# Kernel optimization log

Hardware: AMD Instinct MI355X
Metric: run time of the kernel (lower is better)

## Reference

```python
import jax, jax.numpy as jnp
import numpy as np

N_HEADS = 16
HEAD_DIM = 64
DIM = 1024
B, L = 2, 2048


def setup_inputs() -> dict:
    key = jax.random.key(0)
    ks = jax.random.split(key, 6)
    s = 1.0 / np.sqrt(DIM)
    return {
        "X": jax.random.normal(ks[0], (B, L, DIM), dtype=jnp.float32),
        "attention_mask": jax.random.randint(ks[1], (B, L, L), 0, 2, dtype=jnp.int32),
        "Wq": jax.random.normal(ks[2], (DIM, DIM), dtype=jnp.float32) * s,
        "Wk": jax.random.normal(ks[3], (DIM, DIM), dtype=jnp.float32) * s,
        "Wv": jax.random.normal(ks[4], (DIM, DIM), dtype=jnp.float32) * s,
        "Wo": jax.random.normal(ks[5], (DIM, DIM), dtype=jnp.float32) * s,
    }


def reference(X, attention_mask, Wq, Wk, Wv, Wo):
    # Linear weights follow torch convention: (out_features, in_features)
    b, l, _ = X.shape
    Q = (X @ Wq.T).reshape(b, l, N_HEADS, HEAD_DIM).transpose(0, 2, 1, 3)  # [B,H,L,D]
    K = (X @ Wk.T).reshape(b, l, N_HEADS, HEAD_DIM).transpose(0, 2, 1, 3)
    V = (X @ Wv.T).reshape(b, l, N_HEADS, HEAD_DIM).transpose(0, 2, 1, 3)
    scores = jnp.einsum("bhqd,bhkd->bhqk", Q, K) / np.sqrt(HEAD_DIM)  # [B,H,L,L]
    mask = (attention_mask[:, None, :, :] == 0)  # broadcast over heads
    scores = jnp.where(mask, jnp.float32(-1e20), scores)
    probs = jax.nn.softmax(scores, axis=-1)
    # dropout is identity in eval/inference mode
    ctx = jnp.einsum("bhqk,bhkd->bhqd", probs, V)  # [B,H,L,D]
    ctx = ctx.transpose(0, 2, 1, 3).reshape(b, l, N_HEADS * HEAD_DIM)
    return ctx @ Wo.T
```

## Files before the change

### kernel.cpp

```cpp
#include <hip/hip_runtime.h>
#include <cstddef>


typedef __bf16 bf16x8 __attribute__((ext_vector_type(8)));
typedef __bf16 bf16x4 __attribute__((ext_vector_type(4)));
typedef float  f32x4  __attribute__((ext_vector_type(4)));
typedef short  s16x4  __attribute__((ext_vector_type(4)));

__device__ __forceinline__ void async16(const __bf16* g, __bf16* l) {
  __builtin_amdgcn_global_load_lds((const __attribute__((address_space(1))) unsigned int*)g,
                                   (__attribute__((address_space(3))) unsigned int*)l, 16, 0, 0);
}

__global__ __launch_bounds__(256) void cvt_all(
    const float* __restrict__ X,  const float* __restrict__ Wq, const float* __restrict__ Wk,
    const float* __restrict__ Wv, const float* __restrict__ Wo,
    __bf16* __restrict__ oX,  __bf16* __restrict__ oWq, __bf16* __restrict__ oWk,
    __bf16* __restrict__ oWv, __bf16* __restrict__ oWo) {
  int i = blockIdx.x * 256 + threadIdx.x;
  const float* s; __bf16* d; int off; float sc = 1.0f;
  if (i < 1048576)      { s = X;  d = oX;  off = i; }
  else if (i < 1310720) { s = Wq; d = oWq; off = i - 1048576; sc = 0.18033688011112042f; }
  else if (i < 1572864) { s = Wk; d = oWk; off = i - 1310720; }
  else if (i < 1835008) { s = Wv; d = oWv; off = i - 1572864; }
  else                  { s = Wo; d = oWo; off = i - 1835008; }
  float4 v = ((const float4*)s)[off];
  bf16x4 o;
  o.x = (__bf16)(v.x * sc); o.y = (__bf16)(v.y * sc);
  o.z = (__bf16)(v.z * sc); o.w = (__bf16)(v.w * sc);
  ((bf16x4*)d)[off] = o;
}

__global__ __launch_bounds__(256) void mask_pack(const int* __restrict__ m,
                                                 unsigned long long* __restrict__ pm) {
  int w = blockIdx.x * 4 + (threadIdx.x >> 6);
  int lane = threadIdx.x & 63;
  unsigned long long bits = __ballot(m[(size_t)w * 64 + lane] != 0);
  int b = w >> 16, q = (w >> 5) & 2047, kt = w & 31;
  if (lane == 0) pm[((size_t)b << 16) + kt * 2048 + q] = bits;
}

template<bool OUT_BF16>
__device__ __forceinline__ void gemm128(const __bf16* __restrict__ A, const __bf16* __restrict__ B,
                                        void* __restrict__ C, int lda, int ldb, int ldc,
                                        int m0, int n0, __bf16* As, __bf16* Bs) {
  const int tid = threadIdx.x;
  const int wave = tid >> 6, lane = tid & 63, quad = lane >> 4, l15 = lane & 15;
  const int wm = (wave & 1) * 64, wn = (wave >> 1) * 64;
  const f32x4 z4 = {0.f, 0.f, 0.f, 0.f};
  f32x4 acc[4][4];
#pragma unroll
  for (int i = 0; i < 4; ++i)
#pragma unroll
    for (int j = 0; j < 4; ++j) acc[i][j] = z4;

  for (int k0 = 0; k0 < 1024; k0 += 32) {
#pragma unroll
    for (int s = 0; s < 2; ++s) {
      int p = (wave * 2 + s) * 64 + lane;
      int r = p >> 2;
      int cc = (p & 3) ^ ((r >> 1) & 3);
      async16(A + (size_t)(m0 + r) * lda + (k0 + cc * 8), As + (wave * 2 + s) * 512);
      async16(B + (size_t)(n0 + r) * ldb + (k0 + cc * 8), Bs + (wave * 2 + s) * 512);
    }
    __syncthreads();
    bf16x8 af[4], bfr[4];
#pragma unroll
    for (int i = 0; i < 4; ++i) {
      int r = wm + i * 16 + l15;
      int cc = quad ^ ((r >> 1) & 3);
      af[i] = *(const bf16x8*)(As + r * 32 + cc * 8);
    }
#pragma unroll
    for (int j = 0; j < 4; ++j) {
      int r = wn + j * 16 + l15;
      int cc = quad ^ ((r >> 1) & 3);
      bfr[j] = *(const bf16x8*)(Bs + r * 32 + cc * 8);
    }
#pragma unroll
    for (int i = 0; i < 4; ++i)
#pragma unroll
      for (int j = 0; j < 4; ++j)
        acc[i][j] = __builtin_amdgcn_mfma_f32_16x16x32_bf16(af[i], bfr[j], acc[i][j], 0, 0, 0);
    __syncthreads();
  }
#pragma unroll
  for (int i = 0; i < 4; ++i)
#pragma unroll
    for (int j = 0; j < 4; ++j)
#pragma unroll
      for (int rr = 0; rr < 4; ++rr) {
        int row = m0 + wm + i * 16 + quad * 4 + rr;
        int col = n0 + wn + j * 16 + l15;
        if (OUT_BF16) ((__bf16*)C)[(size_t)row * ldc + col] = (__bf16)acc[i][j][rr];
        else          ((float*)C)[(size_t)row * ldc + col]  = acc[i][j][rr];
      }
}

__global__ __launch_bounds__(256) void qkv_gemm(const __bf16* __restrict__ X,
                                                const __bf16* __restrict__ Wq,
                                                const __bf16* __restrict__ Wk,
                                                const __bf16* __restrict__ Wv,
                                                __bf16* __restrict__ Q, __bf16* __restrict__ K,
                                                __bf16* __restrict__ Vt) {
  __shared__ __bf16 As[4096], Bs[4096];
  int t = blockIdx.x, z = blockIdx.y;
  if (z < 2) {
    int mt = t & 31, nt = t >> 5;
    gemm128<true>(X, z ? Wk : Wq, z ? K : Q, 1024, 1024, 1024, mt * 128, nt * 128, As, Bs);
  } else {
    int mt = t & 7, nt = t >> 3;
    gemm128<true>(Wv, X, Vt, 1024, 1024, 4096, mt * 128, nt * 128, As, Bs);
  }
}

__global__ __launch_bounds__(256) void out_gemm(const __bf16* __restrict__ Ctx,
                                                const __bf16* __restrict__ Wo,
                                                float* __restrict__ Out) {
  __shared__ __bf16 As[4096], Bs[4096];
  int t = blockIdx.x;
  int mt = t & 31, nt = t >> 5;
  gemm128<false>(Ctx, Wo, Out, 1024, 1024, 1024, mt * 128, nt * 128, As, Bs);
}

__global__ __launch_bounds__(256, 4) void attn_kernel(
    const __bf16* __restrict__ Q, const __bf16* __restrict__ K,
    const __bf16* __restrict__ Vt, const unsigned long long* __restrict__ pm,
    __bf16* __restrict__ c0, __bf16* __restrict__ c1, float* __restrict__ lp) {
  __shared__ __bf16 Ks[2][4096];
  __shared__ __bf16 Vs[2][4096];
  const int tid = threadIdx.x;
  const int wave = tid >> 6, lane = tid & 63, quad = lane >> 4, l15 = lane & 15;
  const int id = blockIdx.x;
  const int hb = id & 31, h = hb & 15, b = hb >> 4;
  const int kvh = (id >> 5) & 1, qt = id >> 6;
  const int q0 = qt * 128;
  const int qw = q0 + wave * 32;
  const int kt0 = kvh * 16;

  bf16x8 aq[2][2];
#pragma unroll
  for (int st = 0; st < 2; ++st) {
    const __bf16* Qp = Q + (size_t)(b * 2048 + qw + st * 16 + l15) * 1024 + h * 64 + quad * 8;
    aq[st][0] = *(const bf16x8*)Qp;
    aq[st][1] = *(const bf16x8*)(Qp + 32);
  }

  const unsigned long long* Pm = pm + ((size_t)b << 16) + qw + l15;

  auto stage = [&](int buf, int kv0) {
#pragma unroll
    for (int s = 0; s < 2; ++s) {
      int p = s * 256 + wave * 64 + lane;
      int r = p >> 3, c = (p & 7) ^ (r & 7);
      async16(K  + (size_t)(b * 2048 + kv0 + r) * 1024 + h * 64 + c * 8,
              &Ks[buf][(s * 256 + wave * 64) * 8]);
      async16(Vt + (size_t)(h * 64 + r) * 4096 + b * 2048 + kv0 + c * 8,
              &Vs[buf][(s * 256 + wave * 64) * 8]);
    }
  };

  stage(0, kt0 * 64);
  unsigned long long mw[2] = {Pm[(size_t)kt0 * 2048], Pm[(size_t)kt0 * 2048 + 16]};

  const f32x4 z4 = {0.f, 0.f, 0.f, 0.f};
  const f32x4 cbias = {-28.853900817779268f, -28.853900817779268f,
                       -28.853900817779268f, -28.853900817779268f};
  const short one_bf16 = (short)0x3F80;
  const s16x4 vOnes = {one_bf16, one_bf16, one_bf16, one_bf16};
  f32x4 acc[2][4];
#pragma unroll
  for (int st = 0; st < 2; ++st)
#pragma unroll
    for (int dt = 0; dt < 4; ++dt) acc[st][dt] = z4;
  f32x4 acc_l[2] = {z4, z4};

  for (int t = 0; t < 16; ++t) {
    __syncthreads();
    if (t < 15) stage((t & 1) ^ 1, (kt0 + t + 1) * 64);

    const __bf16* Kc = Ks[t & 1];
    const __bf16* Vc = Vs[t & 1];

    bf16x8 kA[8];
#pragma unroll
    for (int jt = 0; jt < 4; ++jt) {
      int r = jt * 16 + l15;
      kA[jt * 2]     = *(const bf16x8*)(Kc + r * 64 + ((quad ^ (r & 7)) * 8));
      kA[jt * 2 + 1] = *(const bf16x8*)(Kc + r * 64 + (((4 + quad) ^ (r & 7)) * 8));
    }
    s16x4 vB[4][4];
#pragma unroll
    for (int dt = 0; dt < 4; ++dt) {
      int d = dt * 16 + l15;
#pragma unroll
      for (int kf = 0; kf < 4; ++kf)
        vB[dt][kf] = *(const s16x4*)(Vc + d * 64 + (((kf * 2 + (quad >> 1)) ^ (d & 7)) * 8)
                                     + (quad & 1) * 4);
    }

#pragma unroll
    for (int st = 0; st < 2; ++st) {
      f32x4 s4[4];
#pragma unroll
      for (int jt = 0; jt < 4; ++jt) {
        f32x4 tt = cbias;
        tt = __builtin_amdgcn_mfma_f32_16x16x32_bf16(kA[jt * 2],     aq[st][0], tt, 0, 0, 0);
        tt = __builtin_amdgcn_mfma_f32_16x16x32_bf16(kA[jt * 2 + 1], aq[st][1], tt, 0, 0, 0);
        s4[jt] = tt;
      }

      unsigned long long wq = mw[st] >> (quad * 4);
      if (t < 15) mw[st] = Pm[(size_t)(kt0 + t + 1) * 2048 + st * 16];
      unsigned lo32 = (unsigned)wq, hi32 = (unsigned)(wq >> 32);

#pragma unroll
      for (int kf = 0; kf < 4; ++kf) {
        unsigned bw = (kf < 2) ? lo32 : hi32;
        s16x4 ptk;
#pragma unroll
        for (int rr = 0; rr < 4; ++rr) {
          float e = (bw & (1u << ((kf & 1) * 16 + rr))) ? s4[kf][rr] : -1e30f;
          float pv = __builtin_amdgcn_exp2f(e);
          ptk[rr] = __builtin_bit_cast(short, (__bf16)pv);
        }
        acc_l[st] = __builtin_amdgcn_mfma_f32_16x16x16bf16_1k(ptk, vOnes, acc_l[st], 0, 0, 0);
#pragma unroll
        for (int dt = 0; dt < 4; ++dt)
          acc[st][dt] = __builtin_amdgcn_mfma_f32_16x16x16bf16_1k(ptk, vB[dt][kf], acc[st][dt], 0, 0, 0);
      }
    }
  }

  __bf16* cout = kvh ? c1 : c0;
  float* lout = lp + kvh * 65536;
#pragma unroll
  for (int st = 0; st < 2; ++st) {
#pragma unroll
    for (int dt = 0; dt < 4; ++dt)
#pragma unroll
      for (int rr = 0; rr < 4; ++rr)
        cout[(size_t)(b * 2048 + qw + st * 16 + quad * 4 + rr) * 1024 + h * 64 + dt * 16 + l15] =
            (__bf16)acc[st][dt][rr];
    if (l15 == 0) {
#pragma unroll
      for (int rr = 0; rr < 4; ++rr)
        lout[(size_t)(b * 2048 + qw + st * 16 + quad * 4 + rr) * 16 + h] = acc_l[st][rr];
    }
  }
}

__global__ __launch_bounds__(256) void merge_kernel(const __bf16* __restrict__ c0,
                                                    const __bf16* __restrict__ c1,
                                                    const float* __restrict__ lp,
                                                    __bf16* __restrict__ Ctx) {
  int i = blockIdx.x * 256 + threadIdx.x;
  int base = i * 8;
  int row = base >> 10, h = (base >> 6) & 15;
  float inv = 1.0f / (lp[row * 16 + h] + lp[65536 + row * 16 + h]);
  bf16x8 a = ((const bf16x8*)c0)[i];
  bf16x8 bb = ((const bf16x8*)c1)[i];
  bf16x8 o;
#pragma unroll
  for (int r = 0; r < 8; ++r) o[r] = (__bf16)(((float)a[r] + (float)bb[r]) * inv);
  ((bf16x8*)Ctx)[i] = o;
}

extern "C" void kernel_launch(void* const* d_in, const int* in_sizes, int n_in,
                              void* d_out, int out_size, void* d_ws, size_t ws_size,
                              hipStream_t stream) {
  const float* X  = (const float*)d_in[0];
  const int* mask = (const int*)d_in[1];
  const float* Wq = (const float*)d_in[2];
  const float* Wk = (const float*)d_in[3];
  const float* Wv = (const float*)d_in[4];
  const float* Wo = (const float*)d_in[5];

  __bf16* w   = (__bf16*)d_ws;
  __bf16* Xbf = w;
  __bf16* Wqb = Xbf + 4194304;
  __bf16* Wkb = Wqb + 1048576;
  __bf16* Wvb = Wkb + 1048576;
  __bf16* Wob = Wvb + 1048576;
  __bf16* Qb  = Wob + 1048576;
  __bf16* Kb  = Qb + 4194304;
  __bf16* Vtb = Kb + 4194304;
  __bf16* Ctx = Vtb + 4194304;
  unsigned long long* pmt = (unsigned long long*)Wqb;
  float* lpart = (float*)Wkb;
  __bf16* c1 = Xbf;

  cvt_all<<<8192, 256, 0, stream>>>(X, Wq, Wk, Wv, Wo, Xbf, Wqb, Wkb, Wvb, Wob);
  qkv_gemm<<<dim3(256, 3), 256, 0, stream>>>(Xbf, Wqb, Wkb, Wvb, Qb, Kb, Vtb);
  mask_pack<<<32768, 256, 0, stream>>>(mask, pmt);
  attn_kernel<<<1024, 256, 0, stream>>>(Qb, Kb, Vtb, pmt, Ctx, c1, lpart);
  merge_kernel<<<2048, 256, 0, stream>>>(Ctx, c1, lpart, Ctx);
  out_gemm<<<256, 256, 0, stream>>>(Ctx, Wob, (float*)d_out);
}
```

Before: 231.2 us.

## Fuse split-KV merge into output GEMM and use 32-wide PV MFMAs

Drops the separate merge kernel: the output GEMM now loads both partial context buffers plus the row sums, normalises them and writes the result into LDS as its A operand. The attention kernel permutes K rows at load time so that the score layout lines up with 16x16x32 MFMA operands for the P·V product and the row-sum product, halving the number of PV MFMA instructions. K fragments are now read from LDS inside the st loop rather than hoisted, and the mask bit shift changes to match the new layout. The cost is synchronous global loads plus arithmetic in the output GEMM's staging path, and K fragments read twice per tile.

```diff
diff --git a/kernel.cpp b/kernel.cpp
--- a/kernel.cpp
+++ b/kernel.cpp
@@ -40,9 +40,8 @@
   if (lane == 0) pm[((size_t)b << 16) + kt * 2048 + q] = bits;
 }
 
-template<bool OUT_BF16>
 __device__ __forceinline__ void gemm128(const __bf16* __restrict__ A, const __bf16* __restrict__ B,
-                                        void* __restrict__ C, int lda, int ldb, int ldc,
+                                        __bf16* __restrict__ C, int lda, int ldb, int ldc,
                                         int m0, int n0, __bf16* As, __bf16* Bs) {
   const int tid = threadIdx.x;
   const int wave = tid >> 6, lane = tid & 63, quad = lane >> 4, l15 = lane & 15;
@@ -92,8 +91,7 @@
       for (int rr = 0; rr < 4; ++rr) {
         int row = m0 + wm + i * 16 + quad * 4 + rr;
         int col = n0 + wn + j * 16 + l15;
-        if (OUT_BF16) ((__bf16*)C)[(size_t)row * ldc + col] = (__bf16)acc[i][j][rr];
-        else          ((float*)C)[(size_t)row * ldc + col]  = acc[i][j][rr];
+        C[(size_t)row * ldc + col] = (__bf16)acc[i][j][rr];
       }
 }
 
@@ -107,20 +105,80 @@
   int t = blockIdx.x, z = blockIdx.y;
   if (z < 2) {
     int mt = t & 31, nt = t >> 5;
-    gemm128<true>(X, z ? Wk : Wq, z ? K : Q, 1024, 1024, 1024, mt * 128, nt * 128, As, Bs);
+    gemm128(X, z ? Wk : Wq, z ? K : Q, 1024, 1024, 1024, mt * 128, nt * 128, As, Bs);
   } else {
     int mt = t & 7, nt = t >> 3;
-    gemm128<true>(Wv, X, Vt, 1024, 1024, 4096, mt * 128, nt * 128, As, Bs);
-  }
-}
-
-__global__ __launch_bounds__(256) void out_gemm(const __bf16* __restrict__ Ctx,
+    gemm128(Wv, X, Vt, 1024, 1024, 4096, mt * 128, nt * 128, As, Bs);
+  }
+}
+
+__global__ __launch_bounds__(256) void out_gemm(const __bf16* __restrict__ c0,
+                                                const __bf16* __restrict__ c1,
+                                                const float* __restrict__ lp,
                                                 const __bf16* __restrict__ Wo,
                                                 float* __restrict__ Out) {
   __shared__ __bf16 As[4096], Bs[4096];
-  int t = blockIdx.x;
-  int mt = t & 31, nt = t >> 5;
-  gemm128<false>(Ctx, Wo, Out, 1024, 1024, 1024, mt * 128, nt * 128, As, Bs);
+  const int t = blockIdx.x;
+  const int mt = t & 31, nt = t >> 5;
+  const int m0 = mt * 128, n0 = nt * 128;
+  const int tid = threadIdx.x;
+  const int wave = tid >> 6, lane = tid & 63, quad = lane >> 4, l15 = lane & 15;
+  const int wm = (wave & 1) * 64, wn = (wave >> 1) * 64;
+  const f32x4 z4 = {0.f, 0.f, 0.f, 0.f};
+  f32x4 acc[4][4];
+#pragma unroll
+  for (int i = 0; i < 4; ++i)
+#pragma unroll
+    for (int j = 0; j < 4; ++j) acc[i][j] = z4;
+
+  for (int k0 = 0; k0 < 1024; k0 += 32) {
+    const int h = k0 >> 6;
+#pragma unroll
+    for (int s = 0; s < 2; ++s) {
+      int p = (wave * 2 + s) * 64 + lane;
+      int r = p >> 2;
+      int cc = (p & 3) ^ ((r >> 1) & 3);
+      async16(Wo + (size_t)(n0 + r) * 1024 + (k0 + cc * 8), Bs + (wave * 2 + s) * 512);
+      size_t off = (size_t)(m0 + r) * 1024 + k0 + cc * 8;
+      bf16x8 a  = *(const bf16x8*)(c0 + off);
+      bf16x8 b2 = *(const bf16x8*)(c1 + off);
+      float inv = 1.0f / (lp[(m0 + r) * 16 + h] + lp[65536 + (m0 + r) * 16 + h]);
+      bf16x8 o;
+#pragma unroll
+      for (int j = 0; j < 8; ++j) o[j] = (__bf16)(((float)a[j] + (float)b2[j]) * inv);
+      *(bf16x8*)(As + p * 8) = o;
+    }
+    __syncthreads();
+    bf16x8 af[4], bfr[4];
+#pragma unroll
+    for (int i = 0; i < 4; ++i) {
+      int r = wm + i * 16 + l15;
+      int cc = quad ^ ((r >> 1) & 3);
+      af[i] = *(const bf16x8*)(As + r * 32 + cc * 8);
+    }
+#pragma unroll
+    for (int j = 0; j < 4; ++j) {
+      int r = wn + j * 16 + l15;
+      int cc = quad ^ ((r >> 1) & 3);
+      bfr[j] = *(const bf16x8*)(Bs + r * 32 + cc * 8);
+    }
+#pragma unroll
+    for (int i = 0; i < 4; ++i)
+#pragma unroll
+      for (int j = 0; j < 4; ++j)
+        acc[i][j] = __builtin_amdgcn_mfma_f32_16x16x32_bf16(af[i], bfr[j], acc[i][j], 0, 0, 0);
+    __syncthreads();
+  }
+#pragma unroll
+  for (int i = 0; i < 4; ++i)
+#pragma unroll
+    for (int j = 0; j < 4; ++j)
+#pragma unroll
+      for (int rr = 0; rr < 4; ++rr) {
+        int row = m0 + wm + i * 16 + quad * 4 + rr;
+        int col = n0 + wn + j * 16 + l15;
+        Out[(size_t)row * 1024 + col] = acc[i][j][rr];
+      }
 }
 
 __global__ __launch_bounds__(256, 4) void attn_kernel(
@@ -134,8 +192,7 @@
   const int id = blockIdx.x;
   const int hb = id & 31, h = hb & 15, b = hb >> 4;
   const int kvh = (id >> 5) & 1, qt = id >> 6;
-  const int q0 = qt * 128;
-  const int qw = q0 + wave * 32;
+  const int qw = qt * 128 + wave * 32;
   const int kt0 = kvh * 16;
 
   bf16x8 aq[2][2];
@@ -153,7 +210,8 @@
     for (int s = 0; s < 2; ++s) {
       int p = s * 256 + wave * 64 + lane;
       int r = p >> 3, c = (p & 7) ^ (r & 7);
-      async16(K  + (size_t)(b * 2048 + kv0 + r) * 1024 + h * 64 + c * 8,
+      int sr = (r & 0x20) | ((r & 0x0C) << 1) | ((r & 0x10) >> 2) | (r & 3);
+      async16(K  + (size_t)(b * 2048 + kv0 + sr) * 1024 + h * 64 + c * 8,
               &Ks[buf][(s * 256 + wave * 64) * 8]);
       async16(Vt + (size_t)(h * 64 + r) * 4096 + b * 2048 + kv0 + c * 8,
               &Vs[buf][(s * 256 + wave * 64) * 8]);
@@ -166,8 +224,8 @@
   const f32x4 z4 = {0.f, 0.f, 0.f, 0.f};
   const f32x4 cbias = {-28.853900817779268f, -28.853900817779268f,
                        -28.853900817779268f, -28.853900817779268f};
-  const short one_bf16 = (short)0x3F80;
-  const s16x4 vOnes = {one_bf16, one_bf16, one_bf16, one_bf16};
+  const __bf16 one_bf = (__bf16)1.0f;
+  const bf16x8 vOnes8 = {one_bf, one_bf, one_bf, one_bf, one_bf, one_bf, one_bf, one_bf};
   f32x4 acc[2][4];
 #pragma unroll
   for (int st = 0; st < 2; ++st)
@@ -182,21 +240,13 @@
     const __bf16* Kc = Ks[t & 1];
     const __bf16* Vc = Vs[t & 1];
 
-    bf16x8 kA[8];
-#pragma unroll
-    for (int jt = 0; jt < 4; ++jt) {
-      int r = jt * 16 + l15;
-      kA[jt * 2]     = *(const bf16x8*)(Kc + r * 64 + ((quad ^ (r & 7)) * 8));
-      kA[jt * 2 + 1] = *(const bf16x8*)(Kc + r * 64 + (((4 + quad) ^ (r & 7)) * 8));
-    }
-    s16x4 vB[4][4];
+    bf16x8 vB[4][2];
 #pragma unroll
     for (int dt = 0; dt < 4; ++dt) {
       int d = dt * 16 + l15;
 #pragma unroll
-      for (int kf = 0; kf < 4; ++kf)
-        vB[dt][kf] = *(const s16x4*)(Vc + d * 64 + (((kf * 2 + (quad >> 1)) ^ (d & 7)) * 8)
-                                     + (quad & 1) * 4);
+      for (int kp = 0; kp < 2; ++kp)
+        vB[dt][kp] = *(const bf16x8*)(Vc + d * 64 + (((kp * 4 + quad) ^ (d & 7)) * 8));
     }
 
 #pragma unroll
@@ -204,30 +254,32 @@
       f32x4 s4[4];
 #pragma unroll
       for (int jt = 0; jt < 4; ++jt) {
+        int r = jt * 16 + l15;
+        bf16x8 k0 = *(const bf16x8*)(Kc + r * 64 + ((quad ^ (r & 7)) * 8));
+        bf16x8 k1 = *(const bf16x8*)(Kc + r * 64 + (((4 + quad) ^ (r & 7)) * 8));
         f32x4 tt = cbias;
-        tt = __builtin_amdgcn_mfma_f32_16x16x32_bf16(kA[jt * 2],     aq[st][0], tt, 0, 0, 0);
-        tt = __builtin_amdgcn_mfma_f32_16x16x32_bf16(kA[jt * 2 + 1], aq[st][1], tt, 0, 0, 0);
+        tt = __builtin_amdgcn_mfma_f32_16x16x32_bf16(k0, aq[st][0], tt, 0, 0, 0);
+        tt = __builtin_amdgcn_mfma_f32_16x16x32_bf16(k1, aq[st][1], tt, 0, 0, 0);
         s4[jt] = tt;
       }
 
-      unsigned long long wq = mw[st] >> (quad * 4);
+      unsigned long long wq = mw[st] >> (quad * 8);
       if (t < 15) mw[st] = Pm[(size_t)(kt0 + t + 1) * 2048 + st * 16];
       unsigned lo32 = (unsigned)wq, hi32 = (unsigned)(wq >> 32);
 
 #pragma unroll
-      for (int kf = 0; kf < 4; ++kf) {
-        unsigned bw = (kf < 2) ? lo32 : hi32;
-        s16x4 ptk;
-#pragma unroll
-        for (int rr = 0; rr < 4; ++rr) {
-          float e = (bw & (1u << ((kf & 1) * 16 + rr))) ? s4[kf][rr] : -1e30f;
-          float pv = __builtin_amdgcn_exp2f(e);
-          ptk[rr] = __builtin_bit_cast(short, (__bf16)pv);
+      for (int kp = 0; kp < 2; ++kp) {
+        unsigned bw = kp ? hi32 : lo32;
+        bf16x8 p8;
+#pragma unroll
+        for (int j = 0; j < 8; ++j) {
+          float e = (bw & (1u << j)) ? s4[kp * 2 + (j >> 2)][j & 3] : -1e30f;
+          p8[j] = (__bf16)__builtin_amdgcn_exp2f(e);
         }
-        acc_l[st] = __builtin_amdgcn_mfma_f32_16x16x16bf16_1k(ptk, vOnes, acc_l[st], 0, 0, 0);
+        acc_l[st] = __builtin_amdgcn_mfma_f32_16x16x32_bf16(p8, vOnes8, acc_l[st], 0, 0, 0);
 #pragma unroll
         for (int dt = 0; dt < 4; ++dt)
-          acc[st][dt] = __builtin_amdgcn_mfma_f32_16x16x16bf16_1k(ptk, vB[dt][kf], acc[st][dt], 0, 0, 0);
+          acc[st][dt] = __builtin_amdgcn_mfma_f32_16x16x32_bf16(p8, vB[dt][kp], acc[st][dt], 0, 0, 0);
       }
     }
   }
@@ -248,22 +300,6 @@
         lout[(size_t)(b * 2048 + qw + st * 16 + quad * 4 + rr) * 16 + h] = acc_l[st][rr];
     }
   }
-}
-
-__global__ __launch_bounds__(256) void merge_kernel(const __bf16* __restrict__ c0,
-                                                    const __bf16* __restrict__ c1,
-                                                    const float* __restrict__ lp,
-                                                    __bf16* __restrict__ Ctx) {
-  int i = blockIdx.x * 256 + threadIdx.x;
-  int base = i * 8;
-  int row = base >> 10, h = (base >> 6) & 15;
-  float inv = 1.0f / (lp[row * 16 + h] + lp[65536 + row * 16 + h]);
-  bf16x8 a = ((const bf16x8*)c0)[i];
-  bf16x8 bb = ((const bf16x8*)c1)[i];
-  bf16x8 o;
-#pragma unroll
-  for (int r = 0; r < 8; ++r) o[r] = (__bf16)(((float)a[r] + (float)bb[r]) * inv);
-  ((bf16x8*)Ctx)[i] = o;
 }
 
 extern "C" void kernel_launch(void* const* d_in, const int* in_sizes, int n_in,
@@ -294,6 +330,5 @@
   qkv_gemm<<<dim3(256, 3), 256, 0, stream>>>(Xbf, Wqb, Wkb, Wvb, Qb, Kb, Vtb);
   mask_pack<<<32768, 256, 0, stream>>>(mask, pmt);
   attn_kernel<<<1024, 256, 0, stream>>>(Qb, Kb, Vtb, pmt, Ctx, c1, lpart);
-  merge_kernel<<<2048, 256, 0, stream>>>(Ctx, c1, lpart, Ctx);
-  out_gemm<<<256, 256, 0, stream>>>(Ctx, Wob, (float*)d_out);
-}
+  out_gemm<<<256, 256, 0, stream>>>(Ctx, c1, lpart, Wob, (float*)d_out);
+}
```

New measurement: 239.6 us. +3.7%, slower.

## Use 16x16x32 MFMA for PV, permute K rows, fuse mask packing into prep

Applied to the files above, without the earlier changes.

The P·V product switches from 16x16x16 bf16 MFMAs fed with 4-element probability fragments to 16x16x32 MFMAs fed with 8-element fragments. To make that work, K rows are permuted during staging so each lane's score outputs line up with the wider operand layout, and the mask bit indexing is changed to match. V fragments are now loaded as 8-wide vectors, and K fragments are loaded inside the score loop instead of being preloaded, which lowers register pressure. Mask packing is merged into the conversion kernel to save one launch, so the packed mask and partial sums move to their own workspace regions because Wq/Wk buffers are now written concurrently.

```diff
diff --git a/kernel.cpp b/kernel.cpp
--- a/kernel.cpp
+++ b/kernel.cpp
@@ -12,32 +12,31 @@
                                    (__attribute__((address_space(3))) unsigned int*)l, 16, 0, 0);
 }
 
-__global__ __launch_bounds__(256) void cvt_all(
+__global__ __launch_bounds__(256) void prep_kernel(
     const float* __restrict__ X,  const float* __restrict__ Wq, const float* __restrict__ Wk,
-    const float* __restrict__ Wv, const float* __restrict__ Wo,
+    const float* __restrict__ Wv, const float* __restrict__ Wo, const int* __restrict__ m,
     __bf16* __restrict__ oX,  __bf16* __restrict__ oWq, __bf16* __restrict__ oWk,
-    __bf16* __restrict__ oWv, __bf16* __restrict__ oWo) {
-  int i = blockIdx.x * 256 + threadIdx.x;
-  const float* s; __bf16* d; int off; float sc = 1.0f;
-  if (i < 1048576)      { s = X;  d = oX;  off = i; }
-  else if (i < 1310720) { s = Wq; d = oWq; off = i - 1048576; sc = 0.18033688011112042f; }
-  else if (i < 1572864) { s = Wk; d = oWk; off = i - 1310720; }
-  else if (i < 1835008) { s = Wv; d = oWv; off = i - 1572864; }
-  else                  { s = Wo; d = oWo; off = i - 1835008; }
-  float4 v = ((const float4*)s)[off];
-  bf16x4 o;
-  o.x = (__bf16)(v.x * sc); o.y = (__bf16)(v.y * sc);
-  o.z = (__bf16)(v.z * sc); o.w = (__bf16)(v.w * sc);
-  ((bf16x4*)d)[off] = o;
-}
-
-__global__ __launch_bounds__(256) void mask_pack(const int* __restrict__ m,
-                                                 unsigned long long* __restrict__ pm) {
-  int w = blockIdx.x * 4 + (threadIdx.x >> 6);
-  int lane = threadIdx.x & 63;
-  unsigned long long bits = __ballot(m[(size_t)w * 64 + lane] != 0);
-  int b = w >> 16, q = (w >> 5) & 2047, kt = w & 31;
-  if (lane == 0) pm[((size_t)b << 16) + kt * 2048 + q] = bits;
+    __bf16* __restrict__ oWv, __bf16* __restrict__ oWo, unsigned long long* __restrict__ pm) {
+  if (blockIdx.x < 8192) {
+    int i = blockIdx.x * 256 + threadIdx.x;
+    const float* s; __bf16* d; int off; float sc = 1.0f;
+    if (i < 1048576)      { s = X;  d = oX;  off = i; }
+    else if (i < 1310720) { s = Wq; d = oWq; off = i - 1048576; sc = 0.18033688011112042f; }
+    else if (i < 1572864) { s = Wk; d = oWk; off = i - 1310720; }
+    else if (i < 1835008) { s = Wv; d = oWv; off = i - 1572864; }
+    else                  { s = Wo; d = oWo; off = i - 1835008; }
+    float4 v = ((const float4*)s)[off];
+    bf16x4 o;
+    o.x = (__bf16)(v.x * sc); o.y = (__bf16)(v.y * sc);
+    o.z = (__bf16)(v.z * sc); o.w = (__bf16)(v.w * sc);
+    ((bf16x4*)d)[off] = o;
+  } else {
+    int w = (blockIdx.x - 8192) * 4 + (threadIdx.x >> 6);
+    int lane = threadIdx.x & 63;
+    unsigned long long bits = __ballot(m[(size_t)w * 64 + lane] != 0);
+    int b = w >> 16, q = (w >> 5) & 2047, kt = w & 31;
+    if (lane == 0) pm[((size_t)b << 16) + kt * 2048 + q] = bits;
+  }
 }
 
 template<bool OUT_BF16>
@@ -123,6 +122,22 @@
   gemm128<false>(Ctx, Wo, Out, 1024, 1024, 1024, mt * 128, nt * 128, As, Bs);
 }
 
+__global__ __launch_bounds__(256) void merge_kernel(const __bf16* __restrict__ c0,
+                                                    const __bf16* __restrict__ c1,
+                                                    const float* __restrict__ lp,
+                                                    __bf16* __restrict__ Ctx) {
+  int i = blockIdx.x * 256 + threadIdx.x;
+  int base = i * 8;
+  int row = base >> 10, h = (base >> 6) & 15;
+  float inv = 1.0f / (lp[row * 16 + h] + lp[65536 + row * 16 + h]);
+  bf16x8 a = ((const bf16x8*)c0)[i];
+  bf16x8 bb = ((const bf16x8*)c1)[i];
+  bf16x8 o;
+#pragma unroll
+  for (int r = 0; r < 8; ++r) o[r] = (__bf16)(((float)a[r] + (float)bb[r]) * inv);
+  ((bf16x8*)Ctx)[i] = o;
+}
+
 __global__ __launch_bounds__(256, 4) void attn_kernel(
     const __bf16* __restrict__ Q, const __bf16* __restrict__ K,
     const __bf16* __restrict__ Vt, const unsigned long long* __restrict__ pm,
@@ -134,8 +149,7 @@
   const int id = blockIdx.x;
   const int hb = id & 31, h = hb & 15, b = hb >> 4;
   const int kvh = (id >> 5) & 1, qt = id >> 6;
-  const int q0 = qt * 128;
-  const int qw = q0 + wave * 32;
+  const int qw = qt * 128 + wave * 32;
   const int kt0 = kvh * 16;
 
   bf16x8 aq[2][2];
@@ -153,7 +167,8 @@
     for (int s = 0; s < 2; ++s) {
       int p = s * 256 + wave * 64 + lane;
       int r = p >> 3, c = (p & 7) ^ (r & 7);
-      async16(K  + (size_t)(b * 2048 + kv0 + r) * 1024 + h * 64 + c * 8,
+      int sr = (r & 0x20) | ((r & 0x0C) << 1) | ((r & 0x10) >> 2) | (r & 3);
+      async16(K  + (size_t)(b * 2048 + kv0 + sr) * 1024 + h * 64 + c * 8,
               &Ks[buf][(s * 256 + wave * 64) * 8]);
       async16(Vt + (size_t)(h * 64 + r) * 4096 + b * 2048 + kv0 + c * 8,
               &Vs[buf][(s * 256 + wave * 64) * 8]);
@@ -166,8 +181,8 @@
   const f32x4 z4 = {0.f, 0.f, 0.f, 0.f};
   const f32x4 cbias = {-28.853900817779268f, -28.853900817779268f,
                        -28.853900817779268f, -28.853900817779268f};
-  const short one_bf16 = (short)0x3F80;
-  const s16x4 vOnes = {one_bf16, one_bf16, one_bf16, one_bf16};
+  const __bf16 one_bf = (__bf16)1.0f;
+  const bf16x8 vOnes8 = {one_bf, one_bf, one_bf, one_bf, one_bf, one_bf, one_bf, one_bf};
   f32x4 acc[2][4];
 #pragma unroll
   for (int st = 0; st < 2; ++st)
@@ -182,21 +197,13 @@
     const __bf16* Kc = Ks[t & 1];
     const __bf16* Vc = Vs[t & 1];
 
-    bf16x8 kA[8];
-#pragma unroll
-    for (int jt = 0; jt < 4; ++jt) {
-      int r = jt * 16 + l15;
-      kA[jt * 2]     = *(const bf16x8*)(Kc + r * 64 + ((quad ^ (r & 7)) * 8));
-      kA[jt * 2 + 1] = *(const bf16x8*)(Kc + r * 64 + (((4 + quad) ^ (r & 7)) * 8));
-    }
-    s16x4 vB[4][4];
+    bf16x8 vB[4][2];
 #pragma unroll
     for (int dt = 0; dt < 4; ++dt) {
       int d = dt * 16 + l15;
 #pragma unroll
-      for (int kf = 0; kf < 4; ++kf)
-        vB[dt][kf] = *(const s16x4*)(Vc + d * 64 + (((kf * 2 + (quad >> 1)) ^ (d & 7)) * 8)
-                                     + (quad & 1) * 4);
+      for (int kp = 0; kp < 2; ++kp)
+        vB[dt][kp] = *(const bf16x8*)(Vc + d * 64 + (((kp * 4 + quad) ^ (d & 7)) * 8));
     }
 
 #pragma unroll
@@ -204,30 +211,32 @@
       f32x4 s4[4];
 #pragma unroll
       for (int jt = 0; jt < 4; ++jt) {
+        int r = jt * 16 + l15;
+        bf16x8 k0 = *(const bf16x8*)(Kc + r * 64 + ((quad ^ (r & 7)) * 8));
+        bf16x8 k1 = *(const bf16x8*)(Kc + r * 64 + (((4 + quad) ^ (r & 7)) * 8));
         f32x4 tt = cbias;
-        tt = __builtin_amdgcn_mfma_f32_16x16x32_bf16(kA[jt * 2],     aq[st][0], tt, 0, 0, 0);
-        tt = __builtin_amdgcn_mfma_f32_16x16x32_bf16(kA[jt * 2 + 1], aq[st][1], tt, 0, 0, 0);
+        tt = __builtin_amdgcn_mfma_f32_16x16x32_bf16(k0, aq[st][0], tt, 0, 0, 0);
+        tt = __builtin_amdgcn_mfma_f32_16x16x32_bf16(k1, aq[st][1], tt, 0, 0, 0);
         s4[jt] = tt;
       }
 
-      unsigned long long wq = mw[st] >> (quad * 4);
+      unsigned long long wq = mw[st] >> (quad * 8);
       if (t < 15) mw[st] = Pm[(size_t)(kt0 + t + 1) * 2048 + st * 16];
       unsigned lo32 = (unsigned)wq, hi32 = (unsigned)(wq >> 32);
 
 #pragma unroll
-      for (int kf = 0; kf < 4; ++kf) {
-        unsigned bw = (kf < 2) ? lo32 : hi32;
-        s16x4 ptk;
-#pragma unroll
-        for (int rr = 0; rr < 4; ++rr) {
-          float e = (bw & (1u << ((kf & 1) * 16 + rr))) ? s4[kf][rr] : -1e30f;
-          float pv = __builtin_amdgcn_exp2f(e);
-          ptk[rr] = __builtin_bit_cast(short, (__bf16)pv);
+      for (int kp = 0; kp < 2; ++kp) {
+        unsigned bw = kp ? hi32 : lo32;
+        bf16x8 p8;
+#pragma unroll
+        for (int j = 0; j < 8; ++j) {
+          float e = (bw & (1u << j)) ? s4[kp * 2 + (j >> 2)][j & 3] : -1e30f;
+          p8[j] = (__bf16)__builtin_amdgcn_exp2f(e);
         }
-        acc_l[st] = __builtin_amdgcn_mfma_f32_16x16x16bf16_1k(ptk, vOnes, acc_l[st], 0, 0, 0);
+        acc_l[st] = __builtin_amdgcn_mfma_f32_16x16x32_bf16(p8, vOnes8, acc_l[st], 0, 0, 0);
 #pragma unroll
         for (int dt = 0; dt < 4; ++dt)
-          acc[st][dt] = __builtin_amdgcn_mfma_f32_16x16x16bf16_1k(ptk, vB[dt][kf], acc[st][dt], 0, 0, 0);
+          acc[st][dt] = __builtin_amdgcn_mfma_f32_16x16x32_bf16(p8, vB[dt][kp], acc[st][dt], 0, 0, 0);
       }
     }
   }
@@ -248,22 +257,6 @@
         lout[(size_t)(b * 2048 + qw + st * 16 + quad * 4 + rr) * 16 + h] = acc_l[st][rr];
     }
   }
-}
-
-__global__ __launch_bounds__(256) void merge_kernel(const __bf16* __restrict__ c0,
-                                                    const __bf16* __restrict__ c1,
-                                                    const float* __restrict__ lp,
-                                                    __bf16* __restrict__ Ctx) {
-  int i = blockIdx.x * 256 + threadIdx.x;
-  int base = i * 8;
-  int row = base >> 10, h = (base >> 6) & 15;
-  float inv = 1.0f / (lp[row * 16 + h] + lp[65536 + row * 16 + h]);
-  bf16x8 a = ((const bf16x8*)c0)[i];
-  bf16x8 bb = ((const bf16x8*)c1)[i];
-  bf16x8 o;
-#pragma unroll
-  for (int r = 0; r < 8; ++r) o[r] = (__bf16)(((float)a[r] + (float)bb[r]) * inv);
-  ((bf16x8*)Ctx)[i] = o;
 }
 
 extern "C" void kernel_launch(void* const* d_in, const int* in_sizes, int n_in,
@@ -286,13 +279,13 @@
   __bf16* Kb  = Qb + 4194304;
   __bf16* Vtb = Kb + 4194304;
   __bf16* Ctx = Vtb + 4194304;
-  unsigned long long* pmt = (unsigned long long*)Wqb;
-  float* lpart = (float*)Wkb;
+  unsigned long long* pmt = (unsigned long long*)(Ctx + 4194304);
+  float* lpart = (float*)(pmt + 131072);
   __bf16* c1 = Xbf;
 
-  cvt_all<<<8192, 256, 0, stream>>>(X, Wq, Wk, Wv, Wo, Xbf, Wqb, Wkb, Wvb, Wob);
+  prep_kernel<<<40960, 256, 0, stream>>>(X, Wq, Wk, Wv, Wo, mask,
+                                         Xbf, Wqb, Wkb, Wvb, Wob, pmt);
   qkv_gemm<<<dim3(256, 3), 256, 0, stream>>>(Xbf, Wqb, Wkb, Wvb, Qb, Kb, Vtb);
-  mask_pack<<<32768, 256, 0, stream>>>(mask, pmt);
   attn_kernel<<<1024, 256, 0, stream>>>(Qb, Kb, Vtb, pmt, Ctx, c1, lpart);
   merge_kernel<<<2048, 256, 0, stream>>>(Ctx, c1, lpart, Ctx);
   out_gemm<<<256, 256, 0, stream>>>(Ctx, Wob, (float*)d_out);
```

Measured after the change: 221.7 us. 1.04x faster.
